# Performance work log

Hardware: AMD Instinct MI355X
Metric: run time of the kernel (lower is better)

## Reference

```python
import jax, jax.numpy as jnp
import numpy as np
from jax import lax

B, T, I, H = 128, 512, 300, 256


def setup_inputs() -> dict:
    key = jax.random.key(0)
    ks = jax.random.split(key, 10)
    k = 1.0 / np.sqrt(H)
    u = lambda kk, shape: jax.random.uniform(kk, shape, jnp.float32, -k, k)
    return {
        "x": jax.random.normal(ks[0], (B, T, I), jnp.float32),
        "W_ih_f": u(ks[1], (4 * H, I)),
        "W_hh_f": u(ks[2], (4 * H, H)),
        "b_f": u(ks[3], (4 * H,)),
        "W_ih_b": u(ks[4], (4 * H, I)),
        "W_hh_b": u(ks[5], (4 * H, H)),
        "b_b": u(ks[6], (4 * H,)),
        "W_lin": u(ks[7], (2, 2 * H)),
        "b_lin": u(ks[8], (2,)),
    }


def _lstm_dir(x, W_ih, W_hh, b, reverse):
    # Precompute input projections for all timesteps: [B, T, 4H]
    xp = jnp.einsum("bti,gi->btg", x, W_ih) + b
    if reverse:
        xp = xp[:, ::-1]
    h0 = jnp.zeros((x.shape[0], H), x.dtype)
    c0 = jnp.zeros((x.shape[0], H), x.dtype)

    def step(carry, xt):
        h, c = carry
        g = xt + h @ W_hh.T  # [B, 4H]
        i_g, f_g, g_g, o_g = jnp.split(g, 4, axis=-1)  # torch gate order i,f,g,o
        i_g = jax.nn.sigmoid(i_g)
        f_g = jax.nn.sigmoid(f_g)
        g_g = jnp.tanh(g_g)
        o_g = jax.nn.sigmoid(o_g)
        c = f_g * c + i_g * g_g
        h = o_g * jnp.tanh(c)
        return (h, c), h

    _, hs = lax.scan(step, (h0, c0), jnp.swapaxes(xp, 0, 1))  # [T, B, H]
    hs = jnp.swapaxes(hs, 0, 1)  # [B, T, H]
    if reverse:
        hs = hs[:, ::-1]
    return hs


def reference(x, W_ih_f, W_hh_f, b_f, W_ih_b, W_hh_b, b_b, W_lin, b_lin):
    hf = _lstm_dir(x, W_ih_f, W_hh_f, b_f, reverse=False)  # [B, T, H]
    hb = _lstm_dir(x, W_ih_b, W_hh_b, b_b, reverse=True)   # [B, T, H]
    last = jnp.concatenate([hf[:, -1], hb[:, -1]], axis=-1)  # [B, 2H]
    return last @ W_lin.T + b_lin  # [B, 2]
```

## Files before the change

### kernel.cpp

```cpp
#include <hip/hip_runtime.h>
#include <cstdint>
#include <cstddef>

typedef _Float16 half2v __attribute__((ext_vector_type(2)));
typedef _Float16 half4v __attribute__((ext_vector_type(4)));
typedef _Float16 half8v __attribute__((ext_vector_type(8)));
typedef float f32x4 __attribute__((ext_vector_type(4)));

#if __has_builtin(__builtin_amdgcn_fdot2)
#define FDOT2(a, b, c) __builtin_amdgcn_fdot2((a), (b), (c), false)
#else
static __device__ __forceinline__ float fdot2_fb(half2v a, half2v b, float c) {
    return c + (float)a[0] * (float)b[0] + (float)a[1] * (float)b[1];
}
#define FDOT2(a, b, c) fdot2_fb((a), (b), (c))
#endif

__device__ __forceinline__ float sigm(float x) { return 1.0f / (1.0f + __expf(-x)); }
__device__ __forceinline__ float tanh_(float x) { return 1.0f - 2.0f / (__expf(2.0f * x) + 1.0f); }

#define BB 128
#define TT 512
#define II 300
#define IIP 320
#define HH 256
#define GG 1024

__global__ __launch_bounds__(256) void cvt_xw(
    const float* __restrict__ X, const float* __restrict__ W,
    _Float16* __restrict__ Xh, _Float16* __restrict__ Wh)
{
    const int total = (65536 + 1024) * 40;
    for (int c = blockIdx.x * 256 + threadIdx.x; c < total; c += gridDim.x * 256) {
        const int row = c / 40;
        const int ch = c - row * 40;
        const int k0 = ch * 8;
        const float* src;
        _Float16* dst;
        if (row < 65536) {
            src = X + (size_t)row * II;
            dst = Xh + (size_t)row * IIP;
        } else {
            src = W + (size_t)(row - 65536) * II;
            dst = Wh + (size_t)(row - 65536) * IIP;
        }
        half8v hv;
        if (k0 + 8 <= II) {
            float4 a = *(const float4*)(src + k0);
            float4 b = *(const float4*)(src + k0 + 4);
            hv = half8v{(_Float16)a.x, (_Float16)a.y, (_Float16)a.z, (_Float16)a.w,
                        (_Float16)b.x, (_Float16)b.y, (_Float16)b.z, (_Float16)b.w};
        } else {
#pragma unroll
            for (int q = 0; q < 8; ++q) {
                const int k = k0 + q;
                hv[q] = (k < II) ? (_Float16)src[k] : (_Float16)0.f;
            }
        }
        *(half8v*)(dst + k0) = hv;
    }
}

#if __has_builtin(__builtin_amdgcn_global_load_lds)
#define HAVE_GLL 1
__device__ __forceinline__ void gll16(const _Float16* g, _Float16* l) {
    __builtin_amdgcn_global_load_lds(
        (const __attribute__((address_space(1))) void*)g,
        (__attribute__((address_space(3))) void*)l, 16, 0, 0);
}
#else
#define HAVE_GLL 0
#endif

__global__ __launch_bounds__(256) void gemm_xp_h(
    const _Float16* __restrict__ Xh, const _Float16* __restrict__ Wh,
    const float* __restrict__ bias, _Float16* __restrict__ XP)
{
    __shared__ __align__(16) _Float16 As[128 * 32];
    __shared__ __align__(16) _Float16 Bs[128 * 32];

    const int t = threadIdx.x;
    const int m0 = blockIdx.y * 128;
    const int n0 = blockIdx.x * 128;
    const int lane = t & 63;
    const int wv = t >> 6;
    const int mq = (wv >> 1) * 4;
    const int nq = (wv & 1) * 4;

    int rowd[2], k4d[2], cidx[2];
#pragma unroll
    for (int r = 0; r < 2; ++r) {
        const int c = wv * 128 + r * 64 + lane;
        cidx[r] = c;
        rowd[r] = ((c >> 6) << 4) | (c & 15);
        k4d[r] = (c >> 4) & 3;
    }

    f32x4 acc[4][4];
#pragma unroll
    for (int i = 0; i < 4; ++i)
#pragma unroll
        for (int j = 0; j < 4; ++j) acc[i][j] = f32x4{0.f, 0.f, 0.f, 0.f};

    for (int kc = 0; kc < IIP; kc += 32) {
        __syncthreads();
#pragma unroll
        for (int r = 0; r < 2; ++r) {
            const _Float16* ga = Xh + (size_t)(m0 + rowd[r]) * IIP + kc + k4d[r] * 8;
            const _Float16* gb = Wh + (size_t)(n0 + rowd[r]) * IIP + kc + k4d[r] * 8;
#if HAVE_GLL
            gll16(ga, &As[cidx[r] * 8]);
            gll16(gb, &Bs[cidx[r] * 8]);
#else
            *(half8v*)(&As[cidx[r] * 8]) = *(const half8v*)ga;
            *(half8v*)(&Bs[cidx[r] * 8]) = *(const half8v*)gb;
#endif
        }
        __syncthreads();

        half8v af[4], bf[4];
#pragma unroll
        for (int i = 0; i < 4; ++i) {
            af[i] = *(const half8v*)(&As[(mq + i) * 512 + (lane >> 4) * 128 + (lane & 15) * 8]);
            bf[i] = *(const half8v*)(&Bs[(nq + i) * 512 + (lane >> 4) * 128 + (lane & 15) * 8]);
        }
#pragma unroll
        for (int i = 0; i < 4; ++i)
#pragma unroll
            for (int j = 0; j < 4; ++j)
                acc[i][j] = __builtin_amdgcn_mfma_f32_16x16x32_f16(af[i], bf[j], acc[i][j], 0, 0, 0);
    }

#pragma unroll
    for (int j = 0; j < 4; ++j) {
        const int n = n0 + (nq + j) * 16 + (lane & 15);
        const float bv = bias[n];
#pragma unroll
        for (int i = 0; i < 4; ++i) {
#pragma unroll
            for (int r = 0; r < 4; ++r) {
                const int m = m0 + (mq + i) * 16 + (lane >> 4) * 4 + r;
                XP[(size_t)m * GG + n] = (_Float16)(acc[i][j][r] + bv);
            }
        }
    }
}

__global__ __launch_bounds__(256, 3) void gemm_xp(
    const float* __restrict__ X, const float* __restrict__ W,
    const float* __restrict__ bias, _Float16* __restrict__ XP)
{
    __shared__ _Float16 As[128 * 32];
    __shared__ _Float16 Bs[128 * 32];

    const int t = threadIdx.x;
    const int m0 = blockIdx.y * 128;
    const int n0 = blockIdx.x * 128;
    const int kpos = t & 7;
    const int rbase = t >> 3;
    const int lane = t & 63;
    const int wv = t >> 6;
    const int mq = (wv >> 1) * 4;
    const int nq = (wv & 1) * 4;

    f32x4 acc[4][4];
#pragma unroll
    for (int i = 0; i < 4; ++i)
#pragma unroll
        for (int j = 0; j < 4; ++j) acc[i][j] = f32x4{0.f, 0.f, 0.f, 0.f};

    for (int kc = 0; kc < 320; kc += 32) {
        __syncthreads();
        const int k0 = kc + kpos * 4;
#pragma unroll
        for (int rr = 0; rr < 4; ++rr) {
            const int row = rbase + rr * 32;
            float4 va = {0.f, 0.f, 0.f, 0.f}, vb = {0.f, 0.f, 0.f, 0.f};
            if (k0 < 300) {
                va = *(const float4*)(X + (size_t)(m0 + row) * II + k0);
                vb = *(const float4*)(W + (size_t)(n0 + row) * II + k0);
            }
            const int idx = (row >> 4) * 512 + (kpos >> 1) * 128 + (row & 15) * 8 + (kpos & 1) * 4;
            half4v ha = {(_Float16)va.x, (_Float16)va.y, (_Float16)va.z, (_Float16)va.w};
            half4v hb = {(_Float16)vb.x, (_Float16)vb.y, (_Float16)vb.z, (_Float16)vb.w};
            *(half4v*)(&As[idx]) = ha;
            *(half4v*)(&Bs[idx]) = hb;
        }
        __syncthreads();

        half8v af[4], bf[4];
#pragma unroll
        for (int i = 0; i < 4; ++i) {
            af[i] = *(const half8v*)(&As[(mq + i) * 512 + (lane >> 4) * 128 + (lane & 15) * 8]);
            bf[i] = *(const half8v*)(&Bs[(nq + i) * 512 + (lane >> 4) * 128 + (lane & 15) * 8]);
        }
#pragma unroll
        for (int i = 0; i < 4; ++i)
#pragma unroll
            for (int j = 0; j < 4; ++j)
                acc[i][j] = __builtin_amdgcn_mfma_f32_16x16x32_f16(af[i], bf[j], acc[i][j], 0, 0, 0);
    }

#pragma unroll
    for (int j = 0; j < 4; ++j) {
        const int n = n0 + (nq + j) * 16 + (lane & 15);
        const float bv = bias[n];
#pragma unroll
        for (int i = 0; i < 4; ++i) {
#pragma unroll
            for (int r = 0; r < 4; ++r) {
                const int m = m0 + (mq + i) * 16 + (lane >> 4) * 4 + r;
                XP[(size_t)m * GG + n] = (_Float16)(acc[i][j][r] + bv);
            }
        }
    }
}

__global__ __attribute__((amdgpu_flat_work_group_size(512, 512), amdgpu_waves_per_eu(2, 2)))
void lstm_fwd(
    const float* __restrict__ Whh, const _Float16* __restrict__ XP,
    float* __restrict__ HF)
{
    __shared__ _Float16 wlds[8 * GG * 8];
    __shared__ __align__(16) _Float16 hlds[2][HH];

    const int t = threadIdx.x;
    const int b = blockIdx.x;
    const int l = t & 63;
    const int wv = t >> 6;
    const int half = l >> 5;
    const int j = wv * 32 + (l & 31);
    const int row0 = j + (half ? 256 : 0);
    const int row1 = row0 + 512;

    half2v w0[96], w1[96];
#pragma unroll
    for (int i = 0; i < 48; ++i) {
        float4 v = *(const float4*)(Whh + (size_t)row0 * HH + i * 4);
        w0[2 * i]     = half2v{(_Float16)v.x, (_Float16)v.y};
        w0[2 * i + 1] = half2v{(_Float16)v.z, (_Float16)v.w};
    }
#pragma unroll
    for (int i = 0; i < 48; ++i) {
        float4 v = *(const float4*)(Whh + (size_t)row1 * HH + i * 4);
        w1[2 * i]     = half2v{(_Float16)v.x, (_Float16)v.y};
        w1[2 * i + 1] = half2v{(_Float16)v.z, (_Float16)v.w};
    }
#pragma unroll
    for (int grp = 0; grp < 8; ++grp) {
        float4 a  = *(const float4*)(Whh + (size_t)t * HH + 192 + grp * 8);
        float4 c4 = *(const float4*)(Whh + (size_t)t * HH + 192 + grp * 8 + 4);
        half8v hv = {(_Float16)a.x, (_Float16)a.y, (_Float16)a.z, (_Float16)a.w,
                     (_Float16)c4.x, (_Float16)c4.y, (_Float16)c4.z, (_Float16)c4.w};
        *(half8v*)(&wlds[grp * (GG * 8) + t * 8]) = hv;
        float4 a2 = *(const float4*)(Whh + (size_t)(t + 512) * HH + 192 + grp * 8);
        float4 c2 = *(const float4*)(Whh + (size_t)(t + 512) * HH + 192 + grp * 8 + 4);
        half8v hv2 = {(_Float16)a2.x, (_Float16)a2.y, (_Float16)a2.z, (_Float16)a2.w,
                      (_Float16)c2.x, (_Float16)c2.y, (_Float16)c2.z, (_Float16)c2.w};
        *(half8v*)(&wlds[grp * (GG * 8) + (t + 512) * 8]) = hv2;
    }
    if (t < HH) hlds[0][t] = (_Float16)0.f;
    float c = 0.0f;
    __syncthreads();

    const _Float16* xp_b = XP + (size_t)b * TT * GG;
    _Float16 x0 = xp_b[row0];
    _Float16 x1 = xp_b[row1];

    for (int ts = 0; ts < TT; ++ts) {
        const int p = ts & 1;
        const _Float16* hrd = &hlds[p][0];
        const _Float16* xp_n = xp_b + ((ts < TT - 1) ? GG : 0);
        const _Float16 nx0 = xp_n[row0];
        const _Float16 nx1 = xp_n[row1];

        float a0 = 0.f, a1 = 0.f;
#pragma unroll
        for (int cq = 0; cq < 24; ++cq) {
            half8v hv = *(const half8v*)(&hrd[cq * 8]);
            half2v h0 = __builtin_shufflevector(hv, hv, 0, 1);
            half2v h1 = __builtin_shufflevector(hv, hv, 2, 3);
            half2v h2 = __builtin_shufflevector(hv, hv, 4, 5);
            half2v h3 = __builtin_shufflevector(hv, hv, 6, 7);
            a0 = FDOT2(h0, w0[cq * 4 + 0], a0);
            a1 = FDOT2(h0, w1[cq * 4 + 0], a1);
            a0 = FDOT2(h1, w0[cq * 4 + 1], a0);
            a1 = FDOT2(h1, w1[cq * 4 + 1], a1);
            a0 = FDOT2(h2, w0[cq * 4 + 2], a0);
            a1 = FDOT2(h2, w1[cq * 4 + 2], a1);
            a0 = FDOT2(h3, w0[cq * 4 + 3], a0);
            a1 = FDOT2(h3, w1[cq * 4 + 3], a1);
        }
#define LDS_W_STEP(I0, I1)                                                 \
        {                                                                  \
            half2v hp  = __builtin_shufflevector(hv, hv, I0, I1);          \
            half2v wap = __builtin_shufflevector(wa, wa, I0, I1);          \
            half2v wbp = __builtin_shufflevector(wb, wb, I0, I1);          \
            a0 = FDOT2(hp, wap, a0);                                       \
            a1 = FDOT2(hp, wbp, a1);                                       \
        }
#pragma unroll
        for (int grp = 0; grp < 8; ++grp) {
            half8v hv = *(const half8v*)(&hrd[192 + grp * 8]);
            half8v wa = *(const half8v*)(&wlds[grp * (GG * 8) + row0 * 8]);
            half8v wb = *(const half8v*)(&wlds[grp * (GG * 8) + row1 * 8]);
            LDS_W_STEP(0, 1)
            LDS_W_STEP(2, 3)
            LDS_W_STEP(4, 5)
            LDS_W_STEP(6, 7)
        }
#undef LDS_W_STEP
        const float o0 = a0 + (float)x0;
        const float o1 = a1 + (float)x1;
        const float p0 = __shfl_xor(o0, 32, 64);
        const float p1 = __shfl_xor(o1, 32, 64);
        const float gi = half ? p0 : o0;
        const float gg = half ? p1 : o1;
        const float gf = half ? o0 : p0;
        const float go = half ? o1 : p1;
        c = sigm(gf) * c + sigm(gi) * tanh_(gg);
        const float h = sigm(go) * tanh_(c);
        if (!half) {
            hlds[p ^ 1][j] = (_Float16)h;
            if (ts == TT - 1) HF[(size_t)b * HH + j] = h;
        }
        __syncthreads();

        x0 = nx0;
        x1 = nx1;
        xp_b = xp_n;
    }
}

__global__ __launch_bounds__(256) void lstm_bwd(
    const float* __restrict__ X, const float* __restrict__ Wih,
    const float* __restrict__ bb, float* __restrict__ HB)
{
    __shared__ float xs[II];
    const int b = blockIdx.x, t = threadIdx.x;
    const float* xrow = X + ((size_t)b * TT + (TT - 1)) * II;
    if (t < 75) *(float4*)(&xs[t * 4]) = *(const float4*)(xrow + t * 4);
    __syncthreads();
    if (t < HH) {
        float ai = 0.f, ag = 0.f, ao = 0.f;
        const float4* wi = (const float4*)(Wih + (size_t)t * II);
        const float4* wg = (const float4*)(Wih + (size_t)(t + 512) * II);
        const float4* wo = (const float4*)(Wih + (size_t)(t + 768) * II);
        for (int k4 = 0; k4 < 75; ++k4) {
            float4 xv = *(const float4*)(&xs[k4 * 4]);
            float4 a = wi[k4], g4 = wg[k4], o4 = wo[k4];
            ai += xv.x * a.x + xv.y * a.y + xv.z * a.z + xv.w * a.w;
            ag += xv.x * g4.x + xv.y * g4.y + xv.z * g4.z + xv.w * g4.w;
            ao += xv.x * o4.x + xv.y * o4.y + xv.z * o4.z + xv.w * o4.w;
        }
        ai += bb[t];
        ag += bb[t + 512];
        ao += bb[t + 768];
        const float cg = sigm(ai) * tanh_(ag);
        HB[(size_t)b * HH + t] = sigm(ao) * tanh_(cg);
    }
}

__global__ __launch_bounds__(256) void final_k(
    const float* __restrict__ HF, const float* __restrict__ HB,
    const float* __restrict__ Wlin, const float* __restrict__ blin,
    float* __restrict__ OUT)
{
    const int t = threadIdx.x;
    const int b = t >> 1, jj = t & 1;
    float acc = blin[jj];
    const float* wf = Wlin + jj * 512;
    const float* wb = Wlin + jj * 512 + 256;
    const float* hf = HF + (size_t)b * HH;
    const float* hb = HB + (size_t)b * HH;
    for (int k = 0; k < HH; k += 4) {
        float4 h4 = *(const float4*)(hf + k);
        float4 w4 = *(const float4*)(wf + k);
        float4 g4 = *(const float4*)(hb + k);
        float4 v4 = *(const float4*)(wb + k);
        acc += h4.x * w4.x + h4.y * w4.y + h4.z * w4.z + h4.w * w4.w;
        acc += g4.x * v4.x + g4.y * v4.y + g4.z * v4.z + g4.w * v4.w;
    }
    OUT[b * 2 + jj] = acc;
}

extern "C" void kernel_launch(void* const* d_in, const int* in_sizes, int n_in,
                              void* d_out, int out_size, void* d_ws, size_t ws_size,
                              hipStream_t stream)
{
    const float* x = (const float*)d_in[0];
    const float* Wihf = (const float*)d_in[1];
    const float* Whhf = (const float*)d_in[2];
    const float* bf = (const float*)d_in[3];
    const float* Wihb = (const float*)d_in[4];
    const float* Whhb = (const float*)d_in[5];
    const float* bbv = (const float*)d_in[6];
    const float* Wlin = (const float*)d_in[7];
    const float* blin = (const float*)d_in[8];
    float* out = (float*)d_out;
    (void)Whhb; (void)in_sizes; (void)n_in; (void)out_size;

    const size_t XP_B = (size_t)BB * TT * GG * 2;
    const size_t H_B  = (size_t)BB * HH * 4;
    const size_t XH_B = (size_t)65536 * IIP * 2;
    const size_t WH_B = (size_t)GG * IIP * 2;

    _Float16* xp = (_Float16*)d_ws;
    float* hf = (float*)((char*)d_ws + XP_B);
    float* hb = hf + (size_t)BB * HH;
    _Float16* Xh = (_Float16*)((char*)d_ws + XP_B + 2 * H_B);
    _Float16* Wh = Xh + (size_t)65536 * IIP;

    lstm_bwd<<<BB, 256, 0, stream>>>(x, Wihb, bbv, hb);
    if (ws_size >= XP_B + 2 * H_B + XH_B + WH_B) {
        cvt_xw<<<2048, 256, 0, stream>>>(x, Wihf, Xh, Wh);
        gemm_xp_h<<<dim3(GG / 128, (BB * TT) / 128), 256, 0, stream>>>(Xh, Wh, bf, xp);
    } else {
        gemm_xp<<<dim3(GG / 128, (BB * TT) / 128), 256, 0, stream>>>(x, Wihf, bf, xp);
    }
    lstm_fwd<<<BB, 512, 0, stream>>>(Whhf, xp, hf);
    final_k<<<1, 256, 0, stream>>>(hf, hb, Wlin, blin, out);
}
```

Before: 1.241 ms.

## Use one thread per gate row in LSTM recurrence with 1024-thread blocks

Each block of the forward recurrence now runs 1024 threads, and each thread owns a single gate row instead of two. Per-thread register weights drop from two rows to one, and the four gates of a hidden unit are gathered with three cross-lane shuffles. The dot product is split over two accumulators to shorten the FDOT2 dependency chains. This halves per-thread serial work per timestep, but 16 waves now take part in each barrier and every wave makes its own LDS reads of h.

After: 1.538 ms. +23.9%, slower.

```diff
diff --git a/kernel.cpp b/kernel.cpp
--- a/kernel.cpp
+++ b/kernel.cpp
@@ -15,6 +15,8 @@
 }
 #define FDOT2(a, b, c) fdot2_fb((a), (b), (c))
 #endif
+
+#define SV2(v, i0, i1) __builtin_shufflevector((v), (v), (i0), (i1))
 
 __device__ __forceinline__ float sigm(float x) { return 1.0f / (1.0f + __expf(-x)); }
 __device__ __forceinline__ float tanh_(float x) { return 1.0f - 2.0f / (__expf(2.0f * x) + 1.0f); }
@@ -216,35 +218,33 @@
     }
 }
 
-__global__ __attribute__((amdgpu_flat_work_group_size(512, 512), amdgpu_waves_per_eu(2, 2)))
+__global__ __attribute__((amdgpu_flat_work_group_size(1024, 1024), amdgpu_waves_per_eu(4, 4)))
 void lstm_fwd(
     const float* __restrict__ Whh, const _Float16* __restrict__ XP,
     float* __restrict__ HF)
 {
-    __shared__ _Float16 wlds[8 * GG * 8];
+    __shared__ _Float16 wlds[8 * 1024 * 8];
     __shared__ __align__(16) _Float16 hlds[2][HH];
 
     const int t = threadIdx.x;
     const int b = blockIdx.x;
     const int l = t & 63;
     const int wv = t >> 6;
-    const int half = l >> 5;
-    const int j = wv * 32 + (l & 31);
-    const int row0 = j + (half ? 256 : 0);
-    const int row1 = row0 + 512;
-
-    half2v w0[96], w1[96];
-#pragma unroll
-    for (int i = 0; i < 48; ++i) {
-        float4 v = *(const float4*)(Whh + (size_t)row0 * HH + i * 4);
-        w0[2 * i]     = half2v{(_Float16)v.x, (_Float16)v.y};
-        w0[2 * i + 1] = half2v{(_Float16)v.z, (_Float16)v.w};
-    }
-#pragma unroll
-    for (int i = 0; i < 48; ++i) {
-        float4 v = *(const float4*)(Whh + (size_t)row1 * HH + i * 4);
-        w1[2 * i]     = half2v{(_Float16)v.x, (_Float16)v.y};
-        w1[2 * i + 1] = half2v{(_Float16)v.z, (_Float16)v.w};
+    const int gate = l >> 4;
+    const int j = wv * 16 + (l & 15);
+    const int row = gate * 256 + j;
+    const bool gb0 = (gate & 1) != 0;
+    const bool gb1 = (gate & 2) != 0;
+
+    half2v w[96];
+    {
+        const float* wr = Whh + (size_t)row * HH;
+#pragma unroll
+        for (int i = 0; i < 48; ++i) {
+            float4 v = *(const float4*)(wr + i * 4);
+            w[2 * i]     = half2v{(_Float16)v.x, (_Float16)v.y};
+            w[2 * i + 1] = half2v{(_Float16)v.z, (_Float16)v.w};
+        }
     }
 #pragma unroll
     for (int grp = 0; grp < 8; ++grp) {
@@ -252,83 +252,79 @@
         float4 c4 = *(const float4*)(Whh + (size_t)t * HH + 192 + grp * 8 + 4);
         half8v hv = {(_Float16)a.x, (_Float16)a.y, (_Float16)a.z, (_Float16)a.w,
                      (_Float16)c4.x, (_Float16)c4.y, (_Float16)c4.z, (_Float16)c4.w};
-        *(half8v*)(&wlds[grp * (GG * 8) + t * 8]) = hv;
-        float4 a2 = *(const float4*)(Whh + (size_t)(t + 512) * HH + 192 + grp * 8);
-        float4 c2 = *(const float4*)(Whh + (size_t)(t + 512) * HH + 192 + grp * 8 + 4);
-        half8v hv2 = {(_Float16)a2.x, (_Float16)a2.y, (_Float16)a2.z, (_Float16)a2.w,
-                      (_Float16)c2.x, (_Float16)c2.y, (_Float16)c2.z, (_Float16)c2.w};
-        *(half8v*)(&wlds[grp * (GG * 8) + (t + 512) * 8]) = hv2;
+        *(half8v*)(&wlds[grp * 8192 + t * 8]) = hv;
     }
     if (t < HH) hlds[0][t] = (_Float16)0.f;
     float c = 0.0f;
     __syncthreads();
 
-    const _Float16* xp_b = XP + (size_t)b * TT * GG;
-    _Float16 x0 = xp_b[row0];
-    _Float16 x1 = xp_b[row1];
+    const _Float16* xq = XP + (size_t)b * TT * GG + row;
+    _Float16 x = *xq;
 
     for (int ts = 0; ts < TT; ++ts) {
         const int p = ts & 1;
         const _Float16* hrd = &hlds[p][0];
-        const _Float16* xp_n = xp_b + ((ts < TT - 1) ? GG : 0);
-        const _Float16 nx0 = xp_n[row0];
-        const _Float16 nx1 = xp_n[row1];
-
-        float a0 = 0.f, a1 = 0.f;
-#pragma unroll
-        for (int cq = 0; cq < 24; ++cq) {
+        const _Float16* xn = xq + ((ts < TT - 1) ? GG : 0);
+        const _Float16 nx = *xn;
+
+        float aLo = 0.f, aHi = 0.f;
+#pragma unroll
+        for (int cq = 0; cq < 12; ++cq) {
             half8v hv = *(const half8v*)(&hrd[cq * 8]);
-            half2v h0 = __builtin_shufflevector(hv, hv, 0, 1);
-            half2v h1 = __builtin_shufflevector(hv, hv, 2, 3);
-            half2v h2 = __builtin_shufflevector(hv, hv, 4, 5);
-            half2v h3 = __builtin_shufflevector(hv, hv, 6, 7);
-            a0 = FDOT2(h0, w0[cq * 4 + 0], a0);
-            a1 = FDOT2(h0, w1[cq * 4 + 0], a1);
-            a0 = FDOT2(h1, w0[cq * 4 + 1], a0);
-            a1 = FDOT2(h1, w1[cq * 4 + 1], a1);
-            a0 = FDOT2(h2, w0[cq * 4 + 2], a0);
-            a1 = FDOT2(h2, w1[cq * 4 + 2], a1);
-            a0 = FDOT2(h3, w0[cq * 4 + 3], a0);
-            a1 = FDOT2(h3, w1[cq * 4 + 3], a1);
-        }
-#define LDS_W_STEP(I0, I1)                                                 \
-        {                                                                  \
-            half2v hp  = __builtin_shufflevector(hv, hv, I0, I1);          \
-            half2v wap = __builtin_shufflevector(wa, wa, I0, I1);          \
-            half2v wbp = __builtin_shufflevector(wb, wb, I0, I1);          \
-            a0 = FDOT2(hp, wap, a0);                                       \
-            a1 = FDOT2(hp, wbp, a1);                                       \
+            aLo = FDOT2(SV2(hv, 0, 1), w[cq * 4 + 0], aLo);
+            aLo = FDOT2(SV2(hv, 2, 3), w[cq * 4 + 1], aLo);
+            aLo = FDOT2(SV2(hv, 4, 5), w[cq * 4 + 2], aLo);
+            aLo = FDOT2(SV2(hv, 6, 7), w[cq * 4 + 3], aLo);
+        }
+#pragma unroll
+        for (int cq = 12; cq < 24; ++cq) {
+            half8v hv = *(const half8v*)(&hrd[cq * 8]);
+            aHi = FDOT2(SV2(hv, 0, 1), w[cq * 4 + 0], aHi);
+            aHi = FDOT2(SV2(hv, 2, 3), w[cq * 4 + 1], aHi);
+            aHi = FDOT2(SV2(hv, 4, 5), w[cq * 4 + 2], aHi);
+            aHi = FDOT2(SV2(hv, 6, 7), w[cq * 4 + 3], aHi);
         }
 #pragma unroll
         for (int grp = 0; grp < 8; ++grp) {
             half8v hv = *(const half8v*)(&hrd[192 + grp * 8]);
-            half8v wa = *(const half8v*)(&wlds[grp * (GG * 8) + row0 * 8]);
-            half8v wb = *(const half8v*)(&wlds[grp * (GG * 8) + row1 * 8]);
-            LDS_W_STEP(0, 1)
-            LDS_W_STEP(2, 3)
-            LDS_W_STEP(4, 5)
-            LDS_W_STEP(6, 7)
-        }
-#undef LDS_W_STEP
-        const float o0 = a0 + (float)x0;
-        const float o1 = a1 + (float)x1;
-        const float p0 = __shfl_xor(o0, 32, 64);
-        const float p1 = __shfl_xor(o1, 32, 64);
-        const float gi = half ? p0 : o0;
-        const float gg = half ? p1 : o1;
-        const float gf = half ? o0 : p0;
-        const float go = half ? o1 : p1;
+            half8v wl = *(const half8v*)(&wlds[grp * 8192 + row * 8]);
+            if (grp & 1) {
+                aHi = FDOT2(SV2(hv, 0, 1), SV2(wl, 0, 1), aHi);
+                aHi = FDOT2(SV2(hv, 2, 3), SV2(wl, 2, 3), aHi);
+                aHi = FDOT2(SV2(hv, 4, 5), SV2(wl, 4, 5), aHi);
+                aHi = FDOT2(SV2(hv, 6, 7), SV2(wl, 6, 7), aHi);
+            } else {
+                aLo = FDOT2(SV2(hv, 0, 1), SV2(wl, 0, 1), aLo);
+                aLo = FDOT2(SV2(hv, 2, 3), SV2(wl, 2, 3), aLo);
+                aLo = FDOT2(SV2(hv, 4, 5), SV2(wl, 4, 5), aLo);
+                aLo = FDOT2(SV2(hv, 6, 7), SV2(wl, 6, 7), aLo);
+            }
+        }
+
+        const float pre = aLo + aHi + (float)x;
+        const float e1 = __shfl_xor(pre, 16, 64);
+        const float e2 = __shfl_xor(pre, 32, 64);
+        const float e3 = __shfl_xor(pre, 48, 64);
+        const float t01 = gb0 ? e1 : pre;
+        const float t10 = gb0 ? pre : e1;
+        const float t23 = gb0 ? e3 : e2;
+        const float t32 = gb0 ? e2 : e3;
+        const float gi = gb1 ? t23 : t01;
+        const float gf = gb1 ? t32 : t10;
+        const float gg = gb1 ? t01 : t23;
+        const float go = gb1 ? t10 : t32;
+
         c = sigm(gf) * c + sigm(gi) * tanh_(gg);
         const float h = sigm(go) * tanh_(c);
-        if (!half) {
+
+        if (gate == 0) {
             hlds[p ^ 1][j] = (_Float16)h;
             if (ts == TT - 1) HF[(size_t)b * HH + j] = h;
         }
         __syncthreads();
 
-        x0 = nx0;
-        x1 = nx1;
-        xp_b = xp_n;
+        x = nx;
+        xq = xn;
     }
 }
 
@@ -418,6 +414,6 @@
     } else {
         gemm_xp<<<dim3(GG / 128, (BB * TT) / 128), 256, 0, stream>>>(x, Wihf, bf, xp);
     }
-    lstm_fwd<<<BB, 512, 0, stream>>>(Whhf, xp, hf);
+    lstm_fwd<<<BB, 1024, 0, stream>>>(Whhf, xp, hf);
     final_k<<<1, 256, 0, stream>>>(hf, hb, Wlin, blin, out);
 }
```
